# Performance work log

Measured on AMD Instinct MI355X. Metric: run time of the kernel, lower is better.

## Reference

```python
import jax, jax.numpy as jnp
import numpy as np
from jax.ops import segment_sum

N_NODES = 50000
N_EDGES = 800000
IN_DIM, HID_DIM, OUT_DIM = 128, 256, 128


def _glorot(key, shape):
    lim = np.sqrt(6.0 / (shape[0] + shape[1]))
    return jax.random.uniform(key, shape, jnp.float32, -lim, lim)


def setup_inputs() -> dict:
    key = jax.random.key(0)
    ks = jax.random.split(key, 4)
    x = jax.random.normal(ks[0], (N_NODES, IN_DIM), jnp.float32)
    edge_index = jax.random.randint(ks[1], (2, N_EDGES), 0, N_NODES, jnp.int64)
    W1 = _glorot(ks[2], (IN_DIM, HID_DIM))
    b1 = jnp.zeros((HID_DIM,), jnp.float32)
    W2 = _glorot(ks[3], (HID_DIM, OUT_DIM))
    b2 = jnp.zeros((OUT_DIM,), jnp.float32)
    return {"x": x, "edge_index": edge_index, "W1": W1, "b1": b1, "W2": W2, "b2": b2}


def gcn_conv(x, W, b, src, dst, n_nodes):
    # PyG GCNConv: x' = D^{-1/2} (A + I) D^{-1/2} (x W) + b
    h = x @ W  # [N, F_out]
    deg = segment_sum(jnp.ones_like(src, dtype=h.dtype), dst, num_segments=n_nodes) + 1.0  # +1 self loop
    dinv = jax.lax.rsqrt(deg)  # [N]
    norm = dinv[src] * dinv[dst]  # per-edge norm [E]
    msg = h[src] * norm[:, None]  # [E, F_out]
    agg = segment_sum(msg, dst, num_segments=n_nodes)
    agg = agg + h * (dinv * dinv)[:, None]  # self-loop term: norm_ii = dinv_i^2
    return agg + b


def reference(x, edge_index, W1, b1, W2, b2):
    src, dst = edge_index[0], edge_index[1]
    h = gcn_conv(x, W1, b1, src, dst, N_NODES)
    h = jax.nn.relu(h)
    out = gcn_conv(h, W2, b2, src, dst, N_NODES)
    return out
```

## Files before the change

### kernel.cpp

```cpp
#include <hip/hip_runtime.h>

#define N_NODES 50000
#define N_EDGES 800000
#define IN_DIM  128
#define HID_DIM 256
#define OUT_DIM 128
#define BUCKET_CAP 64
#define NCOARSE 196
#define CHUNK 4000
#define NBLK1 200
#define SEGCAP 64
#define HLD 264
#define GROWS 64

typedef __attribute__((ext_vector_type(8))) short short8;
typedef __attribute__((ext_vector_type(4))) float f32x4;

__device__ inline ushort f2b(float f) {
    union { float f; unsigned u; } v; v.f = f;
    return (ushort)((v.u + 0x7FFFu + ((v.u >> 16) & 1u)) >> 16);
}
__device__ inline float b2f(ushort h) {
    union { unsigned u; float f; } v; v.u = ((unsigned)h) << 16;
    return v.f;
}
__device__ inline float2 u2f2(unsigned u) {
    float2 r; r.x = b2f((ushort)(u & 0xFFFFu)); r.y = b2f((ushort)(u >> 16)); return r;
}
__device__ inline unsigned f2u2(float a, float b) {
    return (unsigned)f2b(a) | ((unsigned)f2b(b) << 16);
}
__device__ inline void fma8(float2* acc, uint4 u, float n) {
    float2 v0 = u2f2(u.x), v1 = u2f2(u.y), v2 = u2f2(u.z), v3 = u2f2(u.w);
    acc[0].x += v0.x * n; acc[0].y += v0.y * n;
    acc[1].x += v1.x * n; acc[1].y += v1.y * n;
    acc[2].x += v2.x * n; acc[2].y += v2.y * n;
    acc[3].x += v3.x * n; acc[3].y += v3.y * n;
}


__global__ __launch_bounds__(256) void prep_kernel(const float* __restrict__ x,
                                                   const float* __restrict__ W1,
                                                   const float* __restrict__ W2,
                                                   const int* __restrict__ src,
                                                   const int* __restrict__ dst,
                                                   ushort* __restrict__ xb,
                                                   ushort* __restrict__ w1t,
                                                   ushort* __restrict__ w2t,
                                                   int* __restrict__ bcnt,
                                                   int* __restrict__ binbuf) {
    __shared__ int vals[CHUNK];
    __shared__ ushort lpos[CHUNK];
    __shared__ unsigned char lbin[CHUNK];
    __shared__ int hist[NCOARSE];
    const int b = blockIdx.x;
    const int t = threadIdx.x;
    if (b < 6250) {
        int i = b * 256 + t;
        float4 v = ((const float4*)x)[i];
        ushort4 o; o.x = f2b(v.x); o.y = f2b(v.y); o.z = f2b(v.z); o.w = f2b(v.w);
        ((ushort4*)xb)[i] = o;
    } else if (b < 6506) {
        int i = (b - 6250) * 256 + t;
        if (i < 32768) {
            int n = i >> 7, k = i & 127;
            w1t[i] = f2b(W1[k * HID_DIM + n]);
        } else {
            int j = i - 32768;
            int n = j >> 8, k = j & 255;
            w2t[j] = f2b(W2[k * OUT_DIM + n]);
        }
    } else {
        const int blk = b - 6506;
        const int e0 = blk * CHUNK;
        for (int i = t; i < NCOARSE; i += 256) hist[i] = 0;
        __syncthreads();
        for (int i = t; i < CHUNK; i += 256) {
            int s = src[e0 + i], d = dst[e0 + i];
            int bin = d >> 8;
            vals[i] = (s << 8) | (d & 255);
            lbin[i] = (unsigned char)bin;
            lpos[i] = (ushort)atomicAdd(&hist[bin], 1);
        }
        __syncthreads();
        for (int i = t; i < NCOARSE; i += 256) {
            int h = hist[i]; if (h > SEGCAP) h = SEGCAP;
            bcnt[i * NBLK1 + blk] = h;
        }
        for (int i = t; i < CHUNK; i += 256) {
            int bin = lbin[i];
            int p = lpos[i];
            if (p < SEGCAP) binbuf[((size_t)bin * NBLK1 + blk) * SEGCAP + p] = vals[i];
        }
    }
}


__global__ __launch_bounds__(256) void binpass2_kernel(const int* __restrict__ bcnt,
                                                       const int* __restrict__ binbuf,
                                                       int* __restrict__ cnt,
                                                       float* __restrict__ dinv,
                                                       int* __restrict__ bucket) {
    __shared__ int lcnt[256];
    __shared__ int lm[NBLK1];
    __shared__ int lbuck[256 * BUCKET_CAP];
    const int bin = blockIdx.x;
    const int t = threadIdx.x;
    lcnt[t] = 0;
    if (t < NBLK1) lm[t] = bcnt[bin * NBLK1 + t];
    __syncthreads();
    const int* bb = binbuf + (size_t)bin * NBLK1 * SEGCAP;
    for (int f = t; f < NBLK1 * SEGCAP; f += 256) {
        int blk = f >> 6;
        int sl = f & 63;
        if (sl < lm[blk]) {
            int v = bb[f];
            int dl = v & 255;
            int pos = atomicAdd(&lcnt[dl], 1);
            if (pos < BUCKET_CAP) lbuck[dl * BUCKET_CAP + pos] = v >> 8;
        }
    }
    __syncthreads();
    const int node0 = bin * 256;
    int node = node0 + t;
    if (node < N_NODES) {
        int c = lcnt[t] > BUCKET_CAP ? BUCKET_CAP : lcnt[t];
        cnt[node] = c;
        dinv[node] = rsqrtf((float)c + 1.0f);
    }
    int nvalid = N_NODES - node0; if (nvalid > 256) nvalid = 256;
    if (nvalid <= 0) return;
    int total4 = (nvalid * BUCKET_CAP) >> 2;
    int4* d4 = (int4*)(bucket + (size_t)node0 * BUCKET_CAP);
    const int4* s4 = (const int4*)lbuck;
    for (int j = t; j < total4; j += 256) d4[j] = s4[j];
}


__global__ __launch_bounds__(256) void gather0_kernel(const int* __restrict__ cnt,
                                                      const int* __restrict__ bucket,
                                                      const float* __restrict__ dinv,
                                                      const ushort* __restrict__ xb,
                                                      ushort* __restrict__ aggxb) {
    const int w = blockIdx.x * 4 + (threadIdx.x >> 6);
    const int lane = threadIdx.x & 63;
    const int grp = lane >> 4, sub = lane & 15;
    const int n = cnt[w];
    const float dd = dinv[w];
    int sv = 0; float nv = 0.f;
    if (lane < n) { sv = bucket[w * BUCKET_CAP + lane]; nv = dinv[sv] * dd; }

    float2 acc[4];
    if (grp == 0) {
        uint4 su = ((const uint4*)(xb + (size_t)w * IN_DIM))[sub];
        float sd = dd * dd;
        acc[0] = u2f2(su.x); acc[1] = u2f2(su.y); acc[2] = u2f2(su.z); acc[3] = u2f2(su.w);
#pragma unroll
        for (int j = 0; j < 4; ++j) { acc[j].x *= sd; acc[j].y *= sd; }
    } else {
#pragma unroll
        for (int j = 0; j < 4; ++j) acc[j] = {0.f, 0.f};
    }

    const int nr = (n + 15) & ~15;
    for (int i = 0; i < nr; i += 16) {
        int s0 = __shfl(sv, i + grp),      s1 = __shfl(sv, i + 4 + grp);
        int s2 = __shfl(sv, i + 8 + grp),  s3 = __shfl(sv, i + 12 + grp);
        float n0 = __shfl(nv, i + grp),     n1 = __shfl(nv, i + 4 + grp);
        float n2 = __shfl(nv, i + 8 + grp), n3 = __shfl(nv, i + 12 + grp);
        uint4 u0 = ((const uint4*)(xb + (size_t)s0 * IN_DIM))[sub];
        uint4 u1 = ((const uint4*)(xb + (size_t)s1 * IN_DIM))[sub];
        uint4 u2 = ((const uint4*)(xb + (size_t)s2 * IN_DIM))[sub];
        uint4 u3 = ((const uint4*)(xb + (size_t)s3 * IN_DIM))[sub];
        fma8(acc, u0, n0); fma8(acc, u1, n1); fma8(acc, u2, n2); fma8(acc, u3, n3);
    }
#pragma unroll
    for (int j = 0; j < 4; ++j) {
        acc[j].x += __shfl_down(acc[j].x, 32); acc[j].y += __shfl_down(acc[j].y, 32);
        acc[j].x += __shfl_down(acc[j].x, 16); acc[j].y += __shfl_down(acc[j].y, 16);
    }
    if (lane < 16) {
        uint4 o = {f2u2(acc[0].x, acc[0].y), f2u2(acc[1].x, acc[1].y),
                   f2u2(acc[2].x, acc[2].y), f2u2(acc[3].x, acc[3].y)};
        ((uint4*)(aggxb + (size_t)w * IN_DIM))[sub] = o;
    }
}


__global__ __launch_bounds__(256, 2) void gemm12_mfma(const ushort* __restrict__ aggxb,
                                                      const ushort* __restrict__ w1t,
                                                      const float* __restrict__ b1,
                                                      const ushort* __restrict__ w2t,
                                                      ushort* __restrict__ h2b) {
    __shared__ ushort Hs[GROWS * HLD];
    const int row0 = blockIdx.x * GROWS;
    const int wv = threadIdx.x >> 6;
    const int lane = threadIdx.x & 63;
    const int l15 = lane & 15, q = lane >> 4;

    short8 bf1[16];
#pragma unroll
    for (int kb = 0; kb < 4; ++kb)
#pragma unroll
        for (int t = 0; t < 4; ++t) {
            int col = wv * 64 + t * 16 + l15;
            bf1[kb * 4 + t] = *(const short8*)(w1t + (size_t)col * IN_DIM + kb * 32 + q * 8);
        }
    short8 af[4][4];
#pragma unroll
    for (int sub = 0; sub < 4; ++sub) {
        int ar = row0 + sub * 16 + l15;
        if (ar >= N_NODES) ar = N_NODES - 1;
        const ushort* ab = aggxb + (size_t)ar * IN_DIM + q * 8;
#pragma unroll
        for (int kb = 0; kb < 4; ++kb) af[sub][kb] = *(const short8*)(ab + kb * 32);
    }
    f32x4 acc1[4][4] = {};
#pragma unroll
    for (int sub = 0; sub < 4; ++sub)
#pragma unroll
        for (int kb = 0; kb < 4; ++kb)
#pragma unroll
            for (int t = 0; t < 4; ++t)
                acc1[sub][t] = __builtin_amdgcn_mfma_f32_16x16x32_bf16(
                    af[sub][kb], bf1[kb * 4 + t], acc1[sub][t], 0, 0, 0);
#pragma unroll
    for (int t = 0; t < 4; ++t) {
        int col = wv * 64 + t * 16 + l15;
        float bias = b1[col];
#pragma unroll
        for (int sub = 0; sub < 4; ++sub)
#pragma unroll
            for (int r = 0; r < 4; ++r) {
                int row = sub * 16 + q * 4 + r;
                float v = acc1[sub][t][r] + bias;
                Hs[row * HLD + col] = f2b(v > 0.f ? v : 0.f);
            }
    }
    __syncthreads();

    short8 bf2[16];
#pragma unroll
    for (int kb = 0; kb < 8; ++kb)
#pragma unroll
        for (int t = 0; t < 2; ++t) {
            int col = wv * 32 + t * 16 + l15;
            bf2[kb * 2 + t] = *(const short8*)(w2t + (size_t)col * HID_DIM + kb * 32 + q * 8);
        }
    f32x4 acc2[4][2] = {};
#pragma unroll
    for (int sub = 0; sub < 4; ++sub) {
        const ushort* hb = Hs + (sub * 16 + l15) * HLD + q * 8;
#pragma unroll
        for (int kb = 0; kb < 8; ++kb) {
            short8 a = *(const short8*)(hb + kb * 32);
#pragma unroll
            for (int t = 0; t < 2; ++t)
                acc2[sub][t] = __builtin_amdgcn_mfma_f32_16x16x32_bf16(
                    a, bf2[kb * 2 + t], acc2[sub][t], 0, 0, 0);
        }
    }
#pragma unroll
    for (int sub = 0; sub < 4; ++sub)
#pragma unroll
        for (int t = 0; t < 2; ++t) {
            int col = wv * 32 + t * 16 + l15;
#pragma unroll
            for (int r = 0; r < 4; ++r) {
                int row = row0 + sub * 16 + q * 4 + r;
                if (row < N_NODES)
                    h2b[(size_t)row * OUT_DIM + col] = f2b(acc2[sub][t][r]);
            }
        }
}


__global__ __launch_bounds__(256) void gather2_kernel(const int* __restrict__ cnt,
                                                      const int* __restrict__ bucket,
                                                      const float* __restrict__ dinv,
                                                      const ushort* __restrict__ h2b,
                                                      const float* __restrict__ b2,
                                                      float* __restrict__ out) {
    const int w = blockIdx.x * 4 + (threadIdx.x >> 6);
    const int lane = threadIdx.x & 63;
    const int grp = lane >> 4, sub = lane & 15;
    const int n = cnt[w];
    const float dd = dinv[w];
    int sv = 0; float nv = 0.f;
    if (lane < n) { sv = bucket[w * BUCKET_CAP + lane]; nv = dinv[sv] * dd; }

    float2 acc[4];
    if (grp == 0) {
        uint4 su = ((const uint4*)(h2b + (size_t)w * OUT_DIM))[sub];
        float sd = dd * dd;
        acc[0] = u2f2(su.x); acc[1] = u2f2(su.y); acc[2] = u2f2(su.z); acc[3] = u2f2(su.w);
#pragma unroll
        for (int j = 0; j < 4; ++j) { acc[j].x *= sd; acc[j].y *= sd; }
    } else {
#pragma unroll
        for (int j = 0; j < 4; ++j) acc[j] = {0.f, 0.f};
    }

    const int nr = (n + 15) & ~15;
    for (int i = 0; i < nr; i += 16) {
        int s0 = __shfl(sv, i + grp),      s1 = __shfl(sv, i + 4 + grp);
        int s2 = __shfl(sv, i + 8 + grp),  s3 = __shfl(sv, i + 12 + grp);
        float n0 = __shfl(nv, i + grp),     n1 = __shfl(nv, i + 4 + grp);
        float n2 = __shfl(nv, i + 8 + grp), n3 = __shfl(nv, i + 12 + grp);
        uint4 u0 = ((const uint4*)(h2b + (size_t)s0 * OUT_DIM))[sub];
        uint4 u1 = ((const uint4*)(h2b + (size_t)s1 * OUT_DIM))[sub];
        uint4 u2 = ((const uint4*)(h2b + (size_t)s2 * OUT_DIM))[sub];
        uint4 u3 = ((const uint4*)(h2b + (size_t)s3 * OUT_DIM))[sub];
        fma8(acc, u0, n0); fma8(acc, u1, n1); fma8(acc, u2, n2); fma8(acc, u3, n3);
    }
#pragma unroll
    for (int j = 0; j < 4; ++j) {
        acc[j].x += __shfl_down(acc[j].x, 32); acc[j].y += __shfl_down(acc[j].y, 32);
        acc[j].x += __shfl_down(acc[j].x, 16); acc[j].y += __shfl_down(acc[j].y, 16);
    }
    if (lane < 16) {
        const float4* bp = (const float4*)b2;
        float4 b0 = bp[sub * 2], b1v = bp[sub * 2 + 1];
        float4 o0 = {acc[0].x + b0.x, acc[0].y + b0.y, acc[1].x + b0.z, acc[1].y + b0.w};
        float4 o1 = {acc[2].x + b1v.x, acc[2].y + b1v.y, acc[3].x + b1v.z, acc[3].y + b1v.w};
        float4* op = (float4*)(out + (size_t)w * OUT_DIM);
        op[sub * 2] = o0;
        op[sub * 2 + 1] = o1;
    }
}

extern "C" void kernel_launch(void* const* d_in, const int* in_sizes, int n_in,
                              void* d_out, int out_size, void* d_ws, size_t ws_size,
                              hipStream_t stream) {
    const float* x  = (const float*)d_in[0];
    const int*   ei = (const int*)d_in[1];
    const float* W1 = (const float*)d_in[2];
    const float* b1 = (const float*)d_in[3];
    const float* W2 = (const float*)d_in[4];
    const float* b2 = (const float*)d_in[5];
    float* out = (float*)d_out;

    const int* src = ei;
    const int* dst = ei + N_EDGES;

    char* ws = (char*)d_ws;
    int*    bcnt   = (int*)(ws);
    int*    cnt    = (int*)(ws + 160000);
    float*  dinv   = (float*)(ws + 360000);
    int*    bucket = (int*)(ws + 560000);
    int*    binbuf = (int*)(ws + 13360000);
    ushort* xb     = (ushort*)(ws + 23395200);
    ushort* w1t    = (ushort*)(ws + 36195200);
    ushort* w2t    = (ushort*)(ws + 36260736);
    ushort* aggxb  = (ushort*)(ws + 36326272);
    ushort* h2b    = (ushort*)(ws + 49126272);

    prep_kernel<<<6706, 256, 0, stream>>>(x, W1, W2, src, dst, xb, w1t, w2t, bcnt, binbuf);
    binpass2_kernel<<<NCOARSE, 256, 0, stream>>>(bcnt, binbuf, cnt, dinv, bucket);

    gather0_kernel<<<N_NODES / 4, 256, 0, stream>>>(cnt, bucket, dinv, xb, aggxb);
    gemm12_mfma<<<(N_NODES + GROWS - 1) / GROWS, 256, 0, stream>>>(aggxb, w1t, b1, w2t, h2b);

    gather2_kernel<<<N_NODES / 4, 256, 0, stream>>>(cnt, bucket, dinv, h2b, b2, out);
}
```

Measured before the change: 214.2 us.

## Replace two-pass binned CSR build with direct global atomic bucketing

Removes the two-pass coarse binning (per-chunk shared histogram plus a second bucket-assembly kernel) and instead has each edge thread atomically increment a global per-node counter and write its source into that node's bucket slot. A memset clears the counters first, and dinv is no longer stored but recomputed from cnt inside the gather kernels. This saves a kernel launch and the intermediate binbuf traffic, at the cost of 800k scattered global atomics. Bucket order also becomes nondeterministic, and capped nodes now use the uncapped count for their degree.

```diff
diff --git a/kernel.cpp b/kernel.cpp
--- a/kernel.cpp
+++ b/kernel.cpp
@@ -6,10 +6,6 @@
 #define HID_DIM 256
 #define OUT_DIM 128
 #define BUCKET_CAP 64
-#define NCOARSE 196
-#define CHUNK 4000
-#define NBLK1 200
-#define SEGCAP 64
 #define HLD 264
 #define GROWS 64
 
@@ -47,12 +43,8 @@
                                                    ushort* __restrict__ xb,
                                                    ushort* __restrict__ w1t,
                                                    ushort* __restrict__ w2t,
-                                                   int* __restrict__ bcnt,
-                                                   int* __restrict__ binbuf) {
-    __shared__ int vals[CHUNK];
-    __shared__ ushort lpos[CHUNK];
-    __shared__ unsigned char lbin[CHUNK];
-    __shared__ int hist[NCOARSE];
+                                                   int* __restrict__ cnt,
+                                                   int* __restrict__ bucket) {
     const int b = blockIdx.x;
     const int t = threadIdx.x;
     if (b < 6250) {
@@ -71,84 +63,29 @@
             w2t[j] = f2b(W2[k * OUT_DIM + n]);
         }
     } else {
-        const int blk = b - 6506;
-        const int e0 = blk * CHUNK;
-        for (int i = t; i < NCOARSE; i += 256) hist[i] = 0;
-        __syncthreads();
-        for (int i = t; i < CHUNK; i += 256) {
-            int s = src[e0 + i], d = dst[e0 + i];
-            int bin = d >> 8;
-            vals[i] = (s << 8) | (d & 255);
-            lbin[i] = (unsigned char)bin;
-            lpos[i] = (ushort)atomicAdd(&hist[bin], 1);
-        }
-        __syncthreads();
-        for (int i = t; i < NCOARSE; i += 256) {
-            int h = hist[i]; if (h > SEGCAP) h = SEGCAP;
-            bcnt[i * NBLK1 + blk] = h;
-        }
-        for (int i = t; i < CHUNK; i += 256) {
-            int bin = lbin[i];
-            int p = lpos[i];
-            if (p < SEGCAP) binbuf[((size_t)bin * NBLK1 + blk) * SEGCAP + p] = vals[i];
-        }
-    }
-}
-
-
-__global__ __launch_bounds__(256) void binpass2_kernel(const int* __restrict__ bcnt,
-                                                       const int* __restrict__ binbuf,
-                                                       int* __restrict__ cnt,
-                                                       float* __restrict__ dinv,
-                                                       int* __restrict__ bucket) {
-    __shared__ int lcnt[256];
-    __shared__ int lm[NBLK1];
-    __shared__ int lbuck[256 * BUCKET_CAP];
-    const int bin = blockIdx.x;
-    const int t = threadIdx.x;
-    lcnt[t] = 0;
-    if (t < NBLK1) lm[t] = bcnt[bin * NBLK1 + t];
-    __syncthreads();
-    const int* bb = binbuf + (size_t)bin * NBLK1 * SEGCAP;
-    for (int f = t; f < NBLK1 * SEGCAP; f += 256) {
-        int blk = f >> 6;
-        int sl = f & 63;
-        if (sl < lm[blk]) {
-            int v = bb[f];
-            int dl = v & 255;
-            int pos = atomicAdd(&lcnt[dl], 1);
-            if (pos < BUCKET_CAP) lbuck[dl * BUCKET_CAP + pos] = v >> 8;
-        }
-    }
-    __syncthreads();
-    const int node0 = bin * 256;
-    int node = node0 + t;
-    if (node < N_NODES) {
-        int c = lcnt[t] > BUCKET_CAP ? BUCKET_CAP : lcnt[t];
-        cnt[node] = c;
-        dinv[node] = rsqrtf((float)c + 1.0f);
-    }
-    int nvalid = N_NODES - node0; if (nvalid > 256) nvalid = 256;
-    if (nvalid <= 0) return;
-    int total4 = (nvalid * BUCKET_CAP) >> 2;
-    int4* d4 = (int4*)(bucket + (size_t)node0 * BUCKET_CAP);
-    const int4* s4 = (const int4*)lbuck;
-    for (int j = t; j < total4; j += 256) d4[j] = s4[j];
+        int e = (b - 6506) * 256 + t;
+        int s = src[e], d = dst[e];
+        int p = atomicAdd(&cnt[d], 1);
+        if (p < BUCKET_CAP) bucket[d * BUCKET_CAP + p] = s;
+    }
 }
 
 
 __global__ __launch_bounds__(256) void gather0_kernel(const int* __restrict__ cnt,
                                                       const int* __restrict__ bucket,
-                                                      const float* __restrict__ dinv,
                                                       const ushort* __restrict__ xb,
                                                       ushort* __restrict__ aggxb) {
     const int w = blockIdx.x * 4 + (threadIdx.x >> 6);
     const int lane = threadIdx.x & 63;
     const int grp = lane >> 4, sub = lane & 15;
-    const int n = cnt[w];
-    const float dd = dinv[w];
+    const int ct = cnt[w];
+    const float dd = rsqrtf((float)ct + 1.0f);
+    const int n = ct > BUCKET_CAP ? BUCKET_CAP : ct;
     int sv = 0; float nv = 0.f;
-    if (lane < n) { sv = bucket[w * BUCKET_CAP + lane]; nv = dinv[sv] * dd; }
+    if (lane < n) {
+        sv = bucket[w * BUCKET_CAP + lane];
+        nv = rsqrtf((float)cnt[sv] + 1.0f) * dd;
+    }
 
     float2 acc[4];
     if (grp == 0) {
@@ -277,17 +214,20 @@
 
 __global__ __launch_bounds__(256) void gather2_kernel(const int* __restrict__ cnt,
                                                       const int* __restrict__ bucket,
-                                                      const float* __restrict__ dinv,
                                                       const ushort* __restrict__ h2b,
                                                       const float* __restrict__ b2,
                                                       float* __restrict__ out) {
     const int w = blockIdx.x * 4 + (threadIdx.x >> 6);
     const int lane = threadIdx.x & 63;
     const int grp = lane >> 4, sub = lane & 15;
-    const int n = cnt[w];
-    const float dd = dinv[w];
+    const int ct = cnt[w];
+    const float dd = rsqrtf((float)ct + 1.0f);
+    const int n = ct > BUCKET_CAP ? BUCKET_CAP : ct;
     int sv = 0; float nv = 0.f;
-    if (lane < n) { sv = bucket[w * BUCKET_CAP + lane]; nv = dinv[sv] * dd; }
+    if (lane < n) {
+        sv = bucket[w * BUCKET_CAP + lane];
+        nv = rsqrtf((float)cnt[sv] + 1.0f) * dd;
+    }
 
     float2 acc[4];
     if (grp == 0) {
@@ -344,22 +284,19 @@
     const int* dst = ei + N_EDGES;
 
     char* ws = (char*)d_ws;
-    int*    bcnt   = (int*)(ws);
-    int*    cnt    = (int*)(ws + 160000);
-    float*  dinv   = (float*)(ws + 360000);
-    int*    bucket = (int*)(ws + 560000);
-    int*    binbuf = (int*)(ws + 13360000);
-    ushort* xb     = (ushort*)(ws + 23395200);
-    ushort* w1t    = (ushort*)(ws + 36195200);
-    ushort* w2t    = (ushort*)(ws + 36260736);
-    ushort* aggxb  = (ushort*)(ws + 36326272);
-    ushort* h2b    = (ushort*)(ws + 49126272);
-
-    prep_kernel<<<6706, 256, 0, stream>>>(x, W1, W2, src, dst, xb, w1t, w2t, bcnt, binbuf);
-    binpass2_kernel<<<NCOARSE, 256, 0, stream>>>(bcnt, binbuf, cnt, dinv, bucket);
-
-    gather0_kernel<<<N_NODES / 4, 256, 0, stream>>>(cnt, bucket, dinv, xb, aggxb);
+    int*    cnt    = (int*)(ws);
+    int*    bucket = (int*)(ws + 200000);
+    ushort* xb     = (ushort*)(ws + 13000000);
+    ushort* w1t    = (ushort*)(ws + 25800000);
+    ushort* w2t    = (ushort*)(ws + 25865536);
+    ushort* aggxb  = (ushort*)(ws + 25931072);
+    ushort* h2b    = (ushort*)(ws + 38731072);
+
+    hipMemsetAsync(cnt, 0, N_NODES * sizeof(int), stream);
+    prep_kernel<<<9631, 256, 0, stream>>>(x, W1, W2, src, dst, xb, w1t, w2t, cnt, bucket);
+
+    gather0_kernel<<<N_NODES / 4, 256, 0, stream>>>(cnt, bucket, xb, aggxb);
     gemm12_mfma<<<(N_NODES + GROWS - 1) / GROWS, 256, 0, stream>>>(aggxb, w1t, b1, w2t, h2b);
 
-    gather2_kernel<<<N_NODES / 4, 256, 0, stream>>>(cnt, bucket, dinv, h2b, b2, out);
-}
+    gather2_kernel<<<N_NODES / 4, 256, 0, stream>>>(cnt, bucket, h2b, b2, out);
+}
```

Result: slower. 249.8 us (+16.6%).
